# Kernel optimization log

Measured on AMD Instinct MI355X. Metric: run time of the kernel, lower is better.

The kernel has to match this reference:

```python
import jax, jax.numpy as jnp
import numpy as np

B, S, E, A = 4, 2048, 1024, 1024


def setup_inputs() -> dict:
    key = jax.random.key(0)
    k0, k1, k2, k3 = jax.random.split(key, 4)
    scale = 1.0 / np.sqrt(E)
    return {
        "embeds": jax.random.normal(k0, (B, S, E), dtype=jnp.float32),
        "Wq": jax.random.normal(k1, (E, A), dtype=jnp.float32) * scale,
        "Wk": jax.random.normal(k2, (E, A), dtype=jnp.float32) * scale,
        "Wv": jax.random.normal(k3, (E, A), dtype=jnp.float32) * scale,
    }


def reference(embeds, Wq, Wk, Wv):
    # projections: [B, S, A]
    q = jnp.einsum("bse,ea->bsa", embeds, Wq)
    k = jnp.einsum("bse,ea->bsa", embeds, Wk)
    v = jnp.einsum("bse,ea->bsa", embeds, Wv)
    attn_dim = k.shape[-1]
    # scores: [B, S, S], scaled by sqrt(attention_dim)
    scores = jnp.einsum("bqa,bka->bqk", q, k) / jnp.sqrt(
        jnp.asarray(attn_dim, dtype=q.dtype)
    )
    seq = scores.shape[-1]
    causal = jnp.tril(jnp.ones((seq, seq), dtype=bool))  # [S, S]
    scores = jnp.where(causal[None, :, :], scores, -jnp.inf)
    probs = jax.nn.softmax(scores, axis=-1)
    return jnp.einsum("bqk,bka->bqa", probs, v)
```

## Files before the change

kernel.cpp:

```cpp
#include <hip/hip_runtime.h>
#include <hip/hip_bf16.h>

#define DI __device__ __forceinline__

typedef __attribute__((ext_vector_type(8))) __bf16 bf16x8;
typedef __attribute__((ext_vector_type(4))) float f32x4;
typedef __attribute__((ext_vector_type(8))) short short8;
typedef __attribute__((ext_vector_type(4))) short short4v;
typedef unsigned short u16;

static constexpr int BB = 4, SS = 2048, EE = 1024, AA = 1024;

DI float bf2f(u16 u) { unsigned v = ((unsigned)u) << 16; float f; __builtin_memcpy(&f, &v, 4); return f; }
DI u16 f2bf(float f) { __hip_bfloat16 h = __float2bfloat16(f); u16 u; __builtin_memcpy(&u, &h, 2); return u; }

DI void gload16(const void* g, void* l) {
  __builtin_amdgcn_global_load_lds((const __attribute__((address_space(1))) void*)g,
                                   (__attribute__((address_space(3))) void*)l, 16, 0, 0);
}

DI int xcd_swz(int lin, int nwg) {
  int cpx = nwg >> 3;
  return (lin & 7) * cpx + (lin >> 3);
}

DI bf16x8 read_frag(const char* lds, int R, int c) {
  return *(const bf16x8*)(lds + R * 128 + ((c ^ (R & 7)) << 4));
}

__global__ __launch_bounds__(512, 2) void k_proj5(const u16* __restrict__ Xb, const u16* __restrict__ Wt,
                                                  u16* __restrict__ Qb, u16* __restrict__ Vt) {
  __shared__ __align__(16) char smem[114688];
  const int tid = threadIdx.x, lane = tid & 63, wid = tid >> 6;
  const int wr = wid >> 2, wc = wid & 3;
  const int lane15 = lane & 15, lhi = lane >> 4;
  const int lin = blockIdx.x;
  const int jj = lin >> 3;
  const int mt = (lin & 7) * 4 + (jj & 3);
  const int nt = jj >> 2;
  const u16* Ap = Xb + (size_t)mt * 256 * EE;
  const u16* Bp = Wt + (size_t)nt * 192 * EE;

  auto stageA = [&](int t, char* buf) {
#pragma unroll
    for (int i = 0; i < 4; ++i) {
      int blk = i * 8 + wid;
      int r = blk * 8 + (lane >> 3);
      int c = (lane & 7) ^ (r & 7);
      gload16((const char*)(Ap + (size_t)t * 64 + (size_t)r * EE) + c * 16, buf + blk * 1024);
    }
  };
  auto stageB = [&](int t, char* buf) {
#pragma unroll
    for (int i = 0; i < 3; ++i) {
      int blk = i * 8 + wid;
      int r = blk * 8 + (lane >> 3);
      int c = (lane & 7) ^ (r & 7);
      gload16((const char*)(Bp + (size_t)t * 64 + (size_t)r * EE) + c * 16, buf + 32768 + blk * 1024);
    }
  };

  f32x4 acc[8][3];
#pragma unroll
  for (int i = 0; i < 8; ++i)
#pragma unroll
    for (int j = 0; j < 3; ++j) acc[i][j] = (f32x4)0.f;

  stageA(0, smem); stageB(0, smem);
  asm volatile("s_waitcnt vmcnt(0)" ::: "memory");
  __builtin_amdgcn_s_barrier();

#pragma unroll 1
  for (int t = 0; t < 16; ++t) {
    const char* As = smem + (t & 1) * 57344;
    const char* Bs = As + 32768;
    char* nxt = smem + ((t & 1) ^ 1) * 57344;
    const bool st = (t + 1 < 16);
    bf16x8 bfr[3][2];

#pragma unroll
    for (int q = 0; q < 4; ++q) {
      if (q == 0) {
#pragma unroll
        for (int ni = 0; ni < 3; ++ni)
#pragma unroll
          for (int ks = 0; ks < 2; ++ks)
            bfr[ni][ks] = read_frag(Bs, wc * 48 + ni * 16 + lane15, ks * 4 + lhi);
      }
      bf16x8 af[2][2];
#pragma unroll
      for (int m2 = 0; m2 < 2; ++m2)
#pragma unroll
        for (int ks = 0; ks < 2; ++ks)
          af[m2][ks] = read_frag(As, wr * 128 + (q * 2 + m2) * 16 + lane15, ks * 4 + lhi);
      if (q == 0 && st) stageA(t + 1, nxt);
      if (q == 1 && st) stageB(t + 1, nxt);
      __builtin_amdgcn_s_barrier();
      asm volatile("s_waitcnt lgkmcnt(0)" ::: "memory");
      __builtin_amdgcn_sched_barrier(0);
      __builtin_amdgcn_s_setprio(1);
#pragma unroll
      for (int m2 = 0; m2 < 2; ++m2)
#pragma unroll
        for (int ni = 0; ni < 3; ++ni)
#pragma unroll
          for (int ks = 0; ks < 2; ++ks)
            acc[q * 2 + m2][ni] =
                __builtin_amdgcn_mfma_f32_16x16x32_bf16(af[m2][ks], bfr[ni][ks], acc[q * 2 + m2][ni], 0, 0, 0);
      __builtin_amdgcn_s_setprio(0);
      __builtin_amdgcn_sched_barrier(0);
      if (q == 3) asm volatile("s_waitcnt vmcnt(0)" ::: "memory");
      __builtin_amdgcn_s_barrier();
    }
  }

  const int r0 = mt * 256 + wr * 128;
  const int c0 = nt * 192 + wc * 48;
#pragma unroll
  for (int mi = 0; mi < 8; ++mi) {
    const int grow = r0 + mi * 16 + lhi * 4;
    const int b = grow >> 11, s = grow & 2047;
#pragma unroll
    for (int ni = 0; ni < 3; ++ni) {
      const int col = c0 + ni * 16 + lane15;
      if (col < 2048) {
        u16* base = Qb + (size_t)(col >> 10) * ((size_t)BB * SS * AA);
#pragma unroll
        for (int r = 0; r < 4; ++r)
          base[(size_t)(grow + r) * AA + (col & 1023)] = f2bf(acc[mi][ni][r]);
      } else {
        const int a = col - 2048;
        short4v o;
#pragma unroll
        for (int r = 0; r < 4; ++r) o[r] = (short)f2bf(acc[mi][ni][r]);
        *(short4v*)(Vt + (size_t)b * AA * SS + (size_t)a * SS + s) = o;
      }
    }
  }
}

DI void stage_tile(const u16* g, int ld, char* lds, int wid, int lane) {
#pragma unroll
  for (int i = 0; i < 4; ++i) {
    int blk = i * 4 + wid;
    int r = blk * 8 + (lane >> 3);
    int c = (lane & 7) ^ (r & 7);
    gload16((const char*)(g + (size_t)r * ld) + c * 16, lds + blk * 1024);
  }
}

DI void gemm_tile(const u16* Ap, int lda, const u16* Bp, int ldb, int ksteps,
                  char* smem, f32x4 acc[4][4]) {
  const int tid = threadIdx.x, lane = tid & 63, wid = tid >> 6;
  const int wr = wid >> 1, wc = wid & 1;
  stage_tile(Ap, lda, smem, wid, lane);
  stage_tile(Bp, ldb, smem + 16384, wid, lane);
  asm volatile("s_waitcnt vmcnt(0)" ::: "memory");
  __syncthreads();
#pragma unroll 1
  for (int ks = 0; ks < ksteps; ++ks) {
    const char* As = smem + (ks & 1) * 32768;
    const char* Bs = As + 16384;
    char* nxt = smem + ((ks & 1) ^ 1) * 32768;
    if (ks + 1 < ksteps) {
      stage_tile(Ap + (size_t)(ks + 1) * 64, lda, nxt, wid, lane);
      stage_tile(Bp + (size_t)(ks + 1) * 64, ldb, nxt + 16384, wid, lane);
    }
#pragma unroll
    for (int ksub = 0; ksub < 2; ++ksub) {
      const int c = ksub * 4 + (lane >> 4);
      bf16x8 af[4], bfr[4];
#pragma unroll
      for (int mi = 0; mi < 4; ++mi) af[mi] = read_frag(As, wr * 64 + mi * 16 + (lane & 15), c);
#pragma unroll
      for (int ni = 0; ni < 4; ++ni) bfr[ni] = read_frag(Bs, wc * 64 + ni * 16 + (lane & 15), c);
#pragma unroll
      for (int mi = 0; mi < 4; ++mi)
#pragma unroll
        for (int ni = 0; ni < 4; ++ni)
          acc[mi][ni] = __builtin_amdgcn_mfma_f32_16x16x32_bf16(af[mi], bfr[ni], acc[mi][ni], 0, 0, 0);
    }
    if (ks + 1 < ksteps) asm volatile("s_waitcnt vmcnt(0)" ::: "memory");
    __syncthreads();
  }
}

__global__ __launch_bounds__(256) void k_prep(const float* __restrict__ X, const float* __restrict__ Wq,
                                              const float* __restrict__ Wk, const float* __restrict__ Wv,
                                              u16* __restrict__ Xb, u16* __restrict__ Wt,
                                              float* __restrict__ rowsum) {
  __shared__ float t[64][65];
  const int bid = blockIdx.x;
  if (bid < 8192) {
    if (bid < 32) rowsum[bid * 256 + threadIdx.x] = 0.f;
    size_t i = ((size_t)bid * 256 + threadIdx.x) * 4;
    f32x4 f = *(const f32x4*)(X + i);
    short4v o;
#pragma unroll
    for (int j = 0; j < 4; ++j) o[j] = (short)f2bf(f[j]);
    *(short4v*)(Xb + i) = o;
  } else {
    const int bx = bid - 8192;
    const int w = bx >> 8, rem = bx & 255;
    const int k0 = (rem & 15) * 64, n0 = (rem >> 4) * 64;
    const float* W = (w == 0) ? Wq : ((w == 1) ? Wk : Wv);
    u16* Wo = Wt + (size_t)w * EE * AA;
    const int tx = threadIdx.x & 63, ty = threadIdx.x >> 6;
#pragma unroll
    for (int r = 0; r < 16; ++r) {
      int k = r * 4 + ty;
      t[k][tx] = W[(size_t)(k0 + k) * AA + n0 + tx];
    }
    __syncthreads();
#pragma unroll
    for (int r = 0; r < 16; ++r) {
      int n = r * 4 + ty;
      Wo[(size_t)(n0 + n) * EE + k0 + tx] = f2bf(t[tx][n]);
    }
  }
}

__global__ __launch_bounds__(256) void k_scores(const u16* __restrict__ Q, const u16* __restrict__ K,
                                                u16* __restrict__ Sc, float* __restrict__ rowsum) {
  __shared__ __align__(16) char smem[65536];
  const int wg = xcd_swz(blockIdx.x, 544);
  const int b = wg / 136, t = wg % 136;
  int i = (int)((sqrtf(8.f * t + 1.f) - 1.f) * 0.5f);
  while ((i + 1) * (i + 2) / 2 <= t) ++i;
  while (i * (i + 1) / 2 > t) --i;
  const int j = t - i * (i + 1) / 2;
  const u16* Ap = Q + (size_t)b * SS * AA + (size_t)i * 128 * AA;
  const u16* Bp = K + (size_t)b * SS * AA + (size_t)j * 128 * AA;
  u16* Op = Sc + (size_t)b * SS * SS;
  float* rs = rowsum + (size_t)b * SS;
  f32x4 acc[4][4];
#pragma unroll
  for (int x = 0; x < 4; ++x)
#pragma unroll
    for (int y = 0; y < 4; ++y) acc[x][y] = (f32x4)0.f;
  gemm_tile(Ap, AA, Bp, AA, AA / 64, smem, acc);
  const int lane = threadIdx.x & 63, wid = threadIdx.x >> 6;
  const int r0 = i * 128 + (wid >> 1) * 64, c0 = j * 128 + (wid & 1) * 64;
#pragma unroll
  for (int mi = 0; mi < 4; ++mi)
#pragma unroll
    for (int r = 0; r < 4; ++r) {
      const int row = r0 + mi * 16 + ((lane >> 4) << 2) + r;
      float psum = 0.f;
#pragma unroll
      for (int ni = 0; ni < 4; ++ni) {
        const int col = c0 + ni * 16 + (lane & 15);
        float e = (col <= row) ? __expf(acc[mi][ni][r] * 0.03125f) : 0.f;
        psum += e;
        Op[(size_t)row * SS + col] = f2bf(e);
      }
      psum += __shfl_xor(psum, 1, 16);
      psum += __shfl_xor(psum, 2, 16);
      psum += __shfl_xor(psum, 4, 16);
      psum += __shfl_xor(psum, 8, 16);
      if ((lane & 15) == 0) atomicAdd(&rs[row], psum);
    }
}

__global__ __launch_bounds__(256) void k_pv(const u16* __restrict__ Sc, const u16* __restrict__ Vt,
                                            const float* __restrict__ rowsum, float* __restrict__ Out) {
  __shared__ __align__(16) char smem[65536];
  const int lin = blockIdx.x;
  const int x = lin & 7;
  const int j = lin >> 3;
  const int b = j >> 4, half = (j >> 3) & 1, nt = j & 7;
  const int i = half ? (15 - x) : x;
  const u16* Ap = Sc + (size_t)b * SS * SS + (size_t)i * 128 * SS;
  const u16* Bp = Vt + (size_t)b * AA * SS + (size_t)nt * 128 * SS;
  const float* rs = rowsum + (size_t)b * SS;
  float* Op = Out + (size_t)b * SS * AA;
  f32x4 acc[4][4];
#pragma unroll
  for (int p = 0; p < 4; ++p)
#pragma unroll
    for (int q = 0; q < 4; ++q) acc[p][q] = (f32x4)0.f;
  gemm_tile(Ap, SS, Bp, SS, 2 * (i + 1), smem, acc);
  const int lane = threadIdx.x & 63, wid = threadIdx.x >> 6;
  const int r0 = i * 128 + (wid >> 1) * 64, c0 = nt * 128 + (wid & 1) * 64;
#pragma unroll
  for (int mi = 0; mi < 4; ++mi)
#pragma unroll
    for (int r = 0; r < 4; ++r) {
      const int row = r0 + mi * 16 + ((lane >> 4) << 2) + r;
      const float inv = 1.f / rs[row];
#pragma unroll
      for (int ni = 0; ni < 4; ++ni) {
        const int col = c0 + ni * 16 + (lane & 15);
        Op[(size_t)row * AA + col] = acc[mi][ni][r] * inv;
      }
    }
}

extern "C" void kernel_launch(void* const* d_in, const int* in_sizes, int n_in,
                              void* d_out, int out_size, void* d_ws, size_t ws_size,
                              hipStream_t stream) {
  const float* X  = (const float*)d_in[0];
  const float* Wq = (const float*)d_in[1];
  const float* Wk = (const float*)d_in[2];
  const float* Wv = (const float*)d_in[3];
  float* Out = (float*)d_out;
  char* ws = (char*)d_ws;
  u16* Xb = (u16*)ws;
  u16* Wt = (u16*)(ws + (16u << 20));
  u16* Qb = (u16*)(ws + (22u << 20));
  u16* Kb = (u16*)(ws + (38u << 20));
  u16* Vt = (u16*)(ws + (70u << 20));
  u16* Sc = (u16*)(ws + (86u << 20));
  float* rowsum = (float*)(ws + (118u << 20));

  k_prep<<<dim3(8192 + 768), 256, 0, stream>>>(X, Wq, Wk, Wv, Xb, Wt, rowsum);
  k_proj5<<<dim3(512), 512, 0, stream>>>(Xb, Wt, Qb, Vt);
  k_scores<<<dim3(136 * BB), 256, 0, stream>>>(Qb, Kb, Sc, rowsum);
  k_pv<<<dim3(512), 256, 0, stream>>>(Sc, Vt, rowsum, Out);
}
```

Baseline: 142.8 us.

## Replace 256x192 projection kernel with 128x128 tiles using shared gemm_tile

Drops the hand-pipelined 512-thread projection kernel with 256x192 tiles and ping-pong LDS. In its place is a 256-thread kernel that reuses the generic 128x128 gemm_tile helper across 1536 workgroups, with an XCD-aware tile mapping. The goal is more workgroups and better load balance over the CUs with a simpler code path. The cost is lower per-tile data reuse and the loss of the explicit prefetch/compute overlap and priority scheduling.

```diff
diff --git a/kernel.cpp b/kernel.cpp
--- a/kernel.cpp
+++ b/kernel.cpp
@@ -26,117 +26,6 @@
 
 DI bf16x8 read_frag(const char* lds, int R, int c) {
   return *(const bf16x8*)(lds + R * 128 + ((c ^ (R & 7)) << 4));
-}
-
-__global__ __launch_bounds__(512, 2) void k_proj5(const u16* __restrict__ Xb, const u16* __restrict__ Wt,
-                                                  u16* __restrict__ Qb, u16* __restrict__ Vt) {
-  __shared__ __align__(16) char smem[114688];
-  const int tid = threadIdx.x, lane = tid & 63, wid = tid >> 6;
-  const int wr = wid >> 2, wc = wid & 3;
-  const int lane15 = lane & 15, lhi = lane >> 4;
-  const int lin = blockIdx.x;
-  const int jj = lin >> 3;
-  const int mt = (lin & 7) * 4 + (jj & 3);
-  const int nt = jj >> 2;
-  const u16* Ap = Xb + (size_t)mt * 256 * EE;
-  const u16* Bp = Wt + (size_t)nt * 192 * EE;
-
-  auto stageA = [&](int t, char* buf) {
-#pragma unroll
-    for (int i = 0; i < 4; ++i) {
-      int blk = i * 8 + wid;
-      int r = blk * 8 + (lane >> 3);
-      int c = (lane & 7) ^ (r & 7);
-      gload16((const char*)(Ap + (size_t)t * 64 + (size_t)r * EE) + c * 16, buf + blk * 1024);
-    }
-  };
-  auto stageB = [&](int t, char* buf) {
-#pragma unroll
-    for (int i = 0; i < 3; ++i) {
-      int blk = i * 8 + wid;
-      int r = blk * 8 + (lane >> 3);
-      int c = (lane & 7) ^ (r & 7);
-      gload16((const char*)(Bp + (size_t)t * 64 + (size_t)r * EE) + c * 16, buf + 32768 + blk * 1024);
-    }
-  };
-
-  f32x4 acc[8][3];
-#pragma unroll
-  for (int i = 0; i < 8; ++i)
-#pragma unroll
-    for (int j = 0; j < 3; ++j) acc[i][j] = (f32x4)0.f;
-
-  stageA(0, smem); stageB(0, smem);
-  asm volatile("s_waitcnt vmcnt(0)" ::: "memory");
-  __builtin_amdgcn_s_barrier();
-
-#pragma unroll 1
-  for (int t = 0; t < 16; ++t) {
-    const char* As = smem + (t & 1) * 57344;
-    const char* Bs = As + 32768;
-    char* nxt = smem + ((t & 1) ^ 1) * 57344;
-    const bool st = (t + 1 < 16);
-    bf16x8 bfr[3][2];
-
-#pragma unroll
-    for (int q = 0; q < 4; ++q) {
-      if (q == 0) {
-#pragma unroll
-        for (int ni = 0; ni < 3; ++ni)
-#pragma unroll
-          for (int ks = 0; ks < 2; ++ks)
-            bfr[ni][ks] = read_frag(Bs, wc * 48 + ni * 16 + lane15, ks * 4 + lhi);
-      }
-      bf16x8 af[2][2];
-#pragma unroll
-      for (int m2 = 0; m2 < 2; ++m2)
-#pragma unroll
-        for (int ks = 0; ks < 2; ++ks)
-          af[m2][ks] = read_frag(As, wr * 128 + (q * 2 + m2) * 16 + lane15, ks * 4 + lhi);
-      if (q == 0 && st) stageA(t + 1, nxt);
-      if (q == 1 && st) stageB(t + 1, nxt);
-      __builtin_amdgcn_s_barrier();
-      asm volatile("s_waitcnt lgkmcnt(0)" ::: "memory");
-      __builtin_amdgcn_sched_barrier(0);
-      __builtin_amdgcn_s_setprio(1);
-#pragma unroll
-      for (int m2 = 0; m2 < 2; ++m2)
-#pragma unroll
-        for (int ni = 0; ni < 3; ++ni)
-#pragma unroll
-          for (int ks = 0; ks < 2; ++ks)
-            acc[q * 2 + m2][ni] =
-                __builtin_amdgcn_mfma_f32_16x16x32_bf16(af[m2][ks], bfr[ni][ks], acc[q * 2 + m2][ni], 0, 0, 0);
-      __builtin_amdgcn_s_setprio(0);
-      __builtin_amdgcn_sched_barrier(0);
-      if (q == 3) asm volatile("s_waitcnt vmcnt(0)" ::: "memory");
-      __builtin_amdgcn_s_barrier();
-    }
-  }
-
-  const int r0 = mt * 256 + wr * 128;
-  const int c0 = nt * 192 + wc * 48;
-#pragma unroll
-  for (int mi = 0; mi < 8; ++mi) {
-    const int grow = r0 + mi * 16 + lhi * 4;
-    const int b = grow >> 11, s = grow & 2047;
-#pragma unroll
-    for (int ni = 0; ni < 3; ++ni) {
-      const int col = c0 + ni * 16 + lane15;
-      if (col < 2048) {
-        u16* base = Qb + (size_t)(col >> 10) * ((size_t)BB * SS * AA);
-#pragma unroll
-        for (int r = 0; r < 4; ++r)
-          base[(size_t)(grow + r) * AA + (col & 1023)] = f2bf(acc[mi][ni][r]);
-      } else {
-        const int a = col - 2048;
-        short4v o;
-#pragma unroll
-        for (int r = 0; r < 4; ++r) o[r] = (short)f2bf(acc[mi][ni][r]);
-        *(short4v*)(Vt + (size_t)b * AA * SS + (size_t)a * SS + s) = o;
-      }
-    }
-  }
 }
 
 DI void stage_tile(const u16* g, int ld, char* lds, int wid, int lane) {
@@ -185,6 +74,58 @@
   }
 }
 
+__global__ __launch_bounds__(256) void k_proj8(const u16* __restrict__ Xb, const u16* __restrict__ Wt,
+                                               u16* __restrict__ Qb, u16* __restrict__ Vt) {
+  __shared__ __align__(16) char smem[65536];
+  const int lin = blockIdx.x;
+  const int x = lin & 7;
+  const int jj = lin >> 3;
+  const int nh = jj / 96, rem = jj - nh * 96;
+  const int nt = nh * 12 + (rem >> 3);
+  const int mt = x * 8 + (rem & 7);
+  const u16* Ap = Xb + (size_t)mt * 128 * EE;
+  const u16* Bp = Wt + (size_t)nt * 128 * EE;
+  f32x4 acc[4][4];
+#pragma unroll
+  for (int p = 0; p < 4; ++p)
+#pragma unroll
+    for (int q = 0; q < 4; ++q) acc[p][q] = (f32x4)0.f;
+  gemm_tile(Ap, EE, Bp, EE, EE / 64, smem, acc);
+
+  const int lane = threadIdx.x & 63, wid = threadIdx.x >> 6;
+  const int lane15 = lane & 15, lhi = lane >> 4;
+  const int wr = wid >> 1, wc = wid & 1;
+  const int r0 = mt * 128 + wr * 64;
+  const int c0 = nt * 128 + wc * 64;
+  if (nt < 16) {
+    u16* base = Qb + (size_t)(nt >> 3) * ((size_t)BB * SS * AA);
+    const int cc = c0 & 1023;
+#pragma unroll
+    for (int mi = 0; mi < 4; ++mi)
+#pragma unroll
+      for (int ni = 0; ni < 4; ++ni)
+#pragma unroll
+        for (int r = 0; r < 4; ++r) {
+          int row = r0 + mi * 16 + lhi * 4 + r;
+          base[(size_t)row * AA + cc + ni * 16 + lane15] = f2bf(acc[mi][ni][r]);
+        }
+  } else {
+#pragma unroll
+    for (int mi = 0; mi < 4; ++mi) {
+      const int grow = r0 + mi * 16 + lhi * 4;
+      const int b = grow >> 11, s = grow & 2047;
+#pragma unroll
+      for (int ni = 0; ni < 4; ++ni) {
+        const int a = c0 - 2048 + ni * 16 + lane15;
+        short4v o;
+#pragma unroll
+        for (int r = 0; r < 4; ++r) o[r] = (short)f2bf(acc[mi][ni][r]);
+        *(short4v*)(Vt + (size_t)b * AA * SS + (size_t)a * SS + s) = o;
+      }
+    }
+  }
+}
+
 __global__ __launch_bounds__(256) void k_prep(const float* __restrict__ X, const float* __restrict__ Wq,
                                               const float* __restrict__ Wk, const float* __restrict__ Wv,
                                               u16* __restrict__ Xb, u16* __restrict__ Wt,
@@ -235,9 +176,9 @@
   float* rs = rowsum + (size_t)b * SS;
   f32x4 acc[4][4];
 #pragma unroll
-  for (int x = 0; x < 4; ++x)
-#pragma unroll
-    for (int y = 0; y < 4; ++y) acc[x][y] = (f32x4)0.f;
+  for (int p = 0; p < 4; ++p)
+#pragma unroll
+    for (int q = 0; q < 4; ++q) acc[p][q] = (f32x4)0.f;
   gemm_tile(Ap, AA, Bp, AA, AA / 64, smem, acc);
   const int lane = threadIdx.x & 63, wid = threadIdx.x >> 6;
   const int r0 = i * 128 + (wid >> 1) * 64, c0 = j * 128 + (wid & 1) * 64;
@@ -314,7 +255,7 @@
   float* rowsum = (float*)(ws + (118u << 20));
 
   k_prep<<<dim3(8192 + 768), 256, 0, stream>>>(X, Wq, Wk, Wv, Xb, Wt, rowsum);
-  k_proj5<<<dim3(512), 512, 0, stream>>>(Xb, Wt, Qb, Vt);
+  k_proj8<<<dim3(1536), 256, 0, stream>>>(Xb, Wt, Qb, Vt);
   k_scores<<<dim3(136 * BB), 256, 0, stream>>>(Qb, Kb, Sc, rowsum);
   k_pv<<<dim3(512), 256, 0, stream>>>(Sc, Vt, rowsum, Out);
 }
```

Measured after the change: 141.2 us. About the same (-1.1%).
